# Performance work log

Hardware: AMD Instinct MI355X
Metric: run time of the kernel (lower is better)

The kernel has to match this reference:

```python
import jax, jax.numpy as jnp
import numpy as np

NEG_SLOPE = 0.01  # torch nn.LeakyReLU default


def setup_inputs() -> dict:
    key = jax.random.key(0)
    k1, k2, k3, k4, k5 = jax.random.split(key, 5)
    B, C, N, O = 32, 512, 1024, 512
    x = jax.random.normal(k1, (B, C, N), dtype=jnp.float32)
    wq = jax.random.normal(k2, (C,), dtype=jnp.float32) * (1.0 / np.sqrt(C))
    wk = jax.random.normal(k3, (C,), dtype=jnp.float32) * (1.0 / np.sqrt(C))
    wm = jax.random.normal(k4, (O, C), dtype=jnp.float32) * (1.0 / np.sqrt(C))
    bm = jax.random.normal(k5, (O,), dtype=jnp.float32) * 0.01
    return {"x": x, "wq": wq, "wk": wk, "wm": wm, "bm": bm}


def reference(x, wq, wk, wm, bm):
    # x: [B, C, N]
    q = jnp.einsum('c,bcn->bn', wq, x)            # [B, N] (Conv1d C->1, k=1, no bias)
    k = jnp.einsum('c,bcn->bn', wk, x)            # [B, N]
    scores = q[:, None, :] + k[:, :, None]        # [B, N, N] additive broadcast
    scores = jnp.where(scores > 0, scores, NEG_SLOPE * scores)  # LeakyReLU
    att = jax.nn.softmax(scores, axis=-1)         # softmax over last dim
    agg = jnp.einsum('bcn,bmn->bcm', x, att)      # weighted aggregation [B, C, N]
    out = jnp.einsum('oc,bcm->bom', wm, agg) + bm[None, :, None]  # Conv1d k=1
    return jax.nn.relu(out)
```

## Files before the change

kernel.cpp:

```cpp
#include <hip/hip_runtime.h>


constexpr int B = 32, C = 512, N = 1024, O = 512;
constexpr float L2E = 1.4426950408889634f;

typedef _Float16 half8 __attribute__((ext_vector_type(8)));
typedef _Float16 half4v __attribute__((ext_vector_type(4)));
typedef _Float16 half2v __attribute__((ext_vector_type(2)));
typedef float f32x4 __attribute__((ext_vector_type(4)));

#if __has_builtin(__builtin_amdgcn_exp2f)
#define EXP2(x) __builtin_amdgcn_exp2f(x)
#else
#define EXP2(x) exp2f(x)
#endif

__device__ __forceinline__ half8 cvt8(float4 a, float4 b) {
  half8 h;
  h[0] = (_Float16)a.x; h[1] = (_Float16)a.y; h[2] = (_Float16)a.z; h[3] = (_Float16)a.w;
  h[4] = (_Float16)b.x; h[5] = (_Float16)b.y; h[6] = (_Float16)b.z; h[7] = (_Float16)b.w;
  return h;
}

__global__ __launch_bounds__(256) void gemm_y_kernel(const float* __restrict__ x,
    const float* __restrict__ wm, const float* __restrict__ wq,
    const float* __restrict__ wk, float* __restrict__ q, float* __restrict__ k,
    _Float16* __restrict__ Yt) {
  __shared__ half2v Xs[16 * 130];
  __shared__ __align__(16) _Float16 Ws[128 * 40];
  int b  = blockIdx.y;
  int n0 = blockIdx.x * 128;
  int o0 = blockIdx.z * 128;
  int t = threadIdx.x;
  int w = t >> 6, l = t & 63;
  int nw = w >> 1, ow = w & 1;
  int lm = l & 15, q8 = (l >> 4) * 8, q4 = (l >> 4) * 4;

  int cp = t >> 4, ng = t & 15;
  int wrow = t >> 2, woff = (t & 3) * 8;
  bool doqk = (blockIdx.z == 0);
  float aq[8] = {}, ak[8] = {};

  f32x4 acc[4][4] = {};
  for (int c0 = 0; c0 < C; c0 += 32) {
    const float* xr = x + ((size_t)b * C + c0 + 2 * cp) * N + n0 + ng * 8;
    float4 a0 = *(const float4*)(xr);
    float4 a1 = *(const float4*)(xr + 4);
    float4 b0 = *(const float4*)(xr + N);
    float4 b1 = *(const float4*)(xr + N + 4);
    const float* wr = wm + (size_t)(o0 + wrow) * C + c0 + woff;
    float4 w0 = *(const float4*)(wr);
    float4 w1 = *(const float4*)(wr + 4);
    float4 w2 = *(const float4*)(wr + (size_t)64 * C);
    float4 w3 = *(const float4*)(wr + (size_t)64 * C + 4);

    if (doqk) {
      float2 wq2 = *(const float2*)&wq[c0 + 2 * cp];
      float2 wk2 = *(const float2*)&wk[c0 + 2 * cp];
      aq[0] = fmaf(wq2.x, a0.x, fmaf(wq2.y, b0.x, aq[0]));
      aq[1] = fmaf(wq2.x, a0.y, fmaf(wq2.y, b0.y, aq[1]));
      aq[2] = fmaf(wq2.x, a0.z, fmaf(wq2.y, b0.z, aq[2]));
      aq[3] = fmaf(wq2.x, a0.w, fmaf(wq2.y, b0.w, aq[3]));
      aq[4] = fmaf(wq2.x, a1.x, fmaf(wq2.y, b1.x, aq[4]));
      aq[5] = fmaf(wq2.x, a1.y, fmaf(wq2.y, b1.y, aq[5]));
      aq[6] = fmaf(wq2.x, a1.z, fmaf(wq2.y, b1.z, aq[6]));
      aq[7] = fmaf(wq2.x, a1.w, fmaf(wq2.y, b1.w, aq[7]));
      ak[0] = fmaf(wk2.x, a0.x, fmaf(wk2.y, b0.x, ak[0]));
      ak[1] = fmaf(wk2.x, a0.y, fmaf(wk2.y, b0.y, ak[1]));
      ak[2] = fmaf(wk2.x, a0.z, fmaf(wk2.y, b0.z, ak[2]));
      ak[3] = fmaf(wk2.x, a0.w, fmaf(wk2.y, b0.w, ak[3]));
      ak[4] = fmaf(wk2.x, a1.x, fmaf(wk2.y, b1.x, ak[4]));
      ak[5] = fmaf(wk2.x, a1.y, fmaf(wk2.y, b1.y, ak[5]));
      ak[6] = fmaf(wk2.x, a1.z, fmaf(wk2.y, b1.z, ak[6]));
      ak[7] = fmaf(wk2.x, a1.w, fmaf(wk2.y, b1.w, ak[7]));
    }

    __syncthreads();
    {
      half2v* xp = &Xs[cp * 130 + ng * 8];
      xp[0] = half2v{(_Float16)a0.x, (_Float16)b0.x};
      xp[1] = half2v{(_Float16)a0.y, (_Float16)b0.y};
      xp[2] = half2v{(_Float16)a0.z, (_Float16)b0.z};
      xp[3] = half2v{(_Float16)a0.w, (_Float16)b0.w};
      xp[4] = half2v{(_Float16)a1.x, (_Float16)b1.x};
      xp[5] = half2v{(_Float16)a1.y, (_Float16)b1.y};
      xp[6] = half2v{(_Float16)a1.z, (_Float16)b1.z};
      xp[7] = half2v{(_Float16)a1.w, (_Float16)b1.w};
      *(half8*)&Ws[wrow * 40 + woff]        = cvt8(w0, w1);
      *(half8*)&Ws[(wrow + 64) * 40 + woff] = cvt8(w2, w3);
    }
    __syncthreads();

    half8 af[4], bf[4];
#pragma unroll
    for (int i = 0; i < 4; ++i) {
      int nrow = nw * 64 + i * 16 + lm;
#pragma unroll
      for (int jp = 0; jp < 4; ++jp) {
        half2v p = Xs[(q4 + jp) * 130 + nrow];
        af[i][2 * jp]     = p[0];
        af[i][2 * jp + 1] = p[1];
      }
    }
#pragma unroll
    for (int j = 0; j < 4; ++j)
      bf[j] = *(const half8*)&Ws[(ow * 64 + j * 16 + lm) * 40 + q8];
#pragma unroll
    for (int i = 0; i < 4; ++i)
#pragma unroll
      for (int j = 0; j < 4; ++j)
        acc[i][j] = __builtin_amdgcn_mfma_f32_16x16x32_f16(af[i], bf[j], acc[i][j], 0, 0, 0);
  }

#pragma unroll
  for (int i = 0; i < 4; ++i) {
    int n_b = n0 + nw * 64 + i * 16 + (l >> 4) * 4;
#pragma unroll
    for (int j = 0; j < 4; ++j) {
      int o_c = o0 + ow * 64 + j * 16 + lm;
      half4v h;
      h[0] = (_Float16)acc[i][j][0];
      h[1] = (_Float16)acc[i][j][1];
      h[2] = (_Float16)acc[i][j][2];
      h[3] = (_Float16)acc[i][j][3];
      *(half4v*)&Yt[((size_t)b * O + o_c) * N + n_b] = h;
    }
  }

  if (doqk) {
    float* red = (float*)Ws;
    __syncthreads();
#pragma unroll
    for (int j = 0; j < 8; ++j) red[cp * 132 + ng * 8 + j] = aq[j];
    __syncthreads();
    if (t < 128) {
      float s = 0.f;
#pragma unroll
      for (int p = 0; p < 16; ++p) s += red[p * 132 + t];
      q[b * N + n0 + t] = L2E * s;
    }
    __syncthreads();
#pragma unroll
    for (int j = 0; j < 8; ++j) red[cp * 132 + ng * 8 + j] = ak[j];
    __syncthreads();
    if (t < 128) {
      float s = 0.f;
#pragma unroll
      for (int p = 0; p < 16; ++p) s += red[p * 132 + t];
      k[b * N + n0 + t] = L2E * s;
    }
  }
}

__global__ __launch_bounds__(256) void qmax_kernel(const float* __restrict__ q,
                                                   float* __restrict__ qmax) {
  int b = blockIdx.x;
  int tid = threadIdx.x;
  float m = -1e30f;
  for (int n = tid; n < N; n += 256) m = fmaxf(m, q[b * N + n]);
#pragma unroll
  for (int off = 32; off > 0; off >>= 1) m = fmaxf(m, __shfl_down(m, off, 64));
  __shared__ float red[4];
  if ((tid & 63) == 0) red[tid >> 6] = m;
  __syncthreads();
  if (tid == 0) qmax[b] = fmaxf(fmaxf(red[0], red[1]), fmaxf(red[2], red[3]));
}

__global__ __launch_bounds__(256) void gemm_out_kernel(const _Float16* __restrict__ Yt,
    const float* __restrict__ q, const float* __restrict__ k,
    const float* __restrict__ qmax, const float* __restrict__ bm,
    float* __restrict__ out) {
  __shared__ __align__(16) float qs[N];
  __shared__ float izs[128];
  int b  = blockIdx.y;
  int o0 = blockIdx.x * 128;
  int m0 = blockIdx.z * 128;
  int t = threadIdx.x;
  int w = t >> 6, l = t & 63;
  int mw = w >> 1, ow = w & 1;
  int lm = l & 15, g = l >> 4, q8 = g * 8;

  *(float4*)&qs[t * 4] = *(const float4*)&q[b * N + t * 4];

  float qmv = qmax[b];
  float k2[4], k3[4];
#pragma unroll
  for (int i = 0; i < 4; ++i) {
    float km = k[b * N + m0 + mw * 64 + i * 16 + lm];
    float s0 = qmv + km;
    float M  = fmaxf(s0, 0.01f * s0);
    k2[i] = km - M;
    k3[i] = fmaf(0.01f, km, -M);
  }
  float Zp[4] = {0.f, 0.f, 0.f, 0.f};
  const _Float16* ybase = Yt + ((size_t)b * O + o0 + ow * 64 + lm) * N + q8;
  __syncthreads();

  f32x4 acc[4][4] = {};
#pragma unroll 2
  for (int n0k = 0; n0k < N; n0k += 32) {
    half8 bf[4];
#pragma unroll
    for (int j = 0; j < 4; ++j)
      bf[j] = *(const half8*)(ybase + (size_t)(j * 16) * N + n0k);
    float4 qa = *(const float4*)&qs[n0k + q8];
    float4 qb = *(const float4*)&qs[n0k + q8 + 4];
    float qv[8] = {qa.x, qa.y, qa.z, qa.w, qb.x, qb.y, qb.z, qb.w};
#pragma unroll
    for (int i = 0; i < 4; ++i) {
      half8 af;
      float zz = 0.f;
#pragma unroll
      for (int jj = 0; jj < 8; ++jj) {
        float arg = fmaxf(qv[jj] + k2[i], fmaf(0.01f, qv[jj], k3[i]));
        float e = EXP2(arg);
        zz += e;
        af[jj] = (_Float16)e;
      }
      Zp[i] += zz;
#pragma unroll
      for (int j = 0; j < 4; ++j)
        acc[i][j] = __builtin_amdgcn_mfma_f32_16x16x32_f16(af, bf[j], acc[i][j], 0, 0, 0);
    }
  }

#pragma unroll
  for (int i = 0; i < 4; ++i) {
    float z = Zp[i];
    z += __shfl_xor(z, 16, 64);
    z += __shfl_xor(z, 32, 64);
    if (ow == 0 && g == 0) izs[mw * 64 + i * 16 + lm] = 1.0f / z;
  }
  __syncthreads();

#pragma unroll
  for (int i = 0; i < 4; ++i) {
    int m_b = m0 + mw * 64 + i * 16 + g * 4;
    float4 iz4 = *(const float4*)&izs[mw * 64 + i * 16 + g * 4];
#pragma unroll
    for (int j = 0; j < 4; ++j) {
      int o_c = o0 + ow * 64 + j * 16 + lm;
      float bias = bm[o_c];
      float4 r;
      r.x = fmaxf(fmaf(acc[i][j][0], iz4.x, bias), 0.f);
      r.y = fmaxf(fmaf(acc[i][j][1], iz4.y, bias), 0.f);
      r.z = fmaxf(fmaf(acc[i][j][2], iz4.z, bias), 0.f);
      r.w = fmaxf(fmaf(acc[i][j][3], iz4.w, bias), 0.f);
      *(float4*)&out[((size_t)b * O + o_c) * N + m_b] = r;
    }
  }
}

extern "C" void kernel_launch(void* const* d_in, const int* in_sizes, int n_in,
                              void* d_out, int out_size, void* d_ws, size_t ws_size,
                              hipStream_t stream) {
  const float* x  = (const float*)d_in[0];
  const float* wq = (const float*)d_in[1];
  const float* wk = (const float*)d_in[2];
  const float* wm = (const float*)d_in[3];
  const float* bm = (const float*)d_in[4];
  float* out = (float*)d_out;

  float* q    = (float*)d_ws;
  float* k    = q + B * N;
  float* qmax = k + B * N;
  _Float16* Yt = (_Float16*)(qmax + 64);

  gemm_y_kernel<<<dim3(N / 128, B, O / 128), 256, 0, stream>>>(x, wm, wq, wk, q, k, Yt);
  qmax_kernel<<<dim3(B), 256, 0, stream>>>(q, qmax);
  gemm_out_kernel<<<dim3(O / 128, B, N / 128), 256, 0, stream>>>(Yt, q, k, qmax, bm, out);
}
```

Before: 234.9 us.

## Stage Y tile in shared memory and split waves over m to cut redundant exp work

Changes the wave decomposition from a 2x2 (m,o) split to four waves each owning 32 m-rows across all 128 o-columns. Each exp/softmax weight is now computed once per block rather than twice, halving the transcendental work. The Y tile is staged cooperatively through padded shared memory each k-step, which adds two barriers per iteration and LDS traffic. The normalizer now sums the fp16-rounded weights so it matches what the MFMAs consume.

```diff
diff --git a/kernel.cpp b/kernel.cpp
--- a/kernel.cpp
+++ b/kernel.cpp
@@ -171,75 +171,84 @@
     const float* __restrict__ qmax, const float* __restrict__ bm,
     float* __restrict__ out) {
   __shared__ __align__(16) float qs[N];
+  __shared__ __align__(16) _Float16 Ys[128 * 40];
   __shared__ float izs[128];
   int b  = blockIdx.y;
   int o0 = blockIdx.x * 128;
   int m0 = blockIdx.z * 128;
   int t = threadIdx.x;
   int w = t >> 6, l = t & 63;
-  int mw = w >> 1, ow = w & 1;
   int lm = l & 15, g = l >> 4, q8 = g * 8;
 
   *(float4*)&qs[t * 4] = *(const float4*)&q[b * N + t * 4];
 
   float qmv = qmax[b];
-  float k2[4], k3[4];
-#pragma unroll
-  for (int i = 0; i < 4; ++i) {
-    float km = k[b * N + m0 + mw * 64 + i * 16 + lm];
+  float k2[2], k3[2];
+#pragma unroll
+  for (int i = 0; i < 2; ++i) {
+    float km = k[b * N + m0 + w * 32 + i * 16 + lm];
     float s0 = qmv + km;
     float M  = fmaxf(s0, 0.01f * s0);
     k2[i] = km - M;
     k3[i] = fmaf(0.01f, km, -M);
   }
-  float Zp[4] = {0.f, 0.f, 0.f, 0.f};
-  const _Float16* ybase = Yt + ((size_t)b * O + o0 + ow * 64 + lm) * N + q8;
+  float Zp[2] = {0.f, 0.f};
+  int yr = t >> 1, yp = t & 1;
+  const _Float16* ysrc = Yt + ((size_t)b * O + o0 + yr) * N + yp * 16;
   __syncthreads();
 
-  f32x4 acc[4][4] = {};
-#pragma unroll 2
+  f32x4 acc[2][8] = {};
   for (int n0k = 0; n0k < N; n0k += 32) {
-    half8 bf[4];
-#pragma unroll
-    for (int j = 0; j < 4; ++j)
-      bf[j] = *(const half8*)(ybase + (size_t)(j * 16) * N + n0k);
+    half8 y0 = *(const half8*)(ysrc + n0k);
+    half8 y1 = *(const half8*)(ysrc + n0k + 8);
     float4 qa = *(const float4*)&qs[n0k + q8];
     float4 qb = *(const float4*)&qs[n0k + q8 + 4];
     float qv[8] = {qa.x, qa.y, qa.z, qa.w, qb.x, qb.y, qb.z, qb.w};
-#pragma unroll
-    for (int i = 0; i < 4; ++i) {
-      half8 af;
+    half8 af[2];
+#pragma unroll
+    for (int i = 0; i < 2; ++i) {
       float zz = 0.f;
 #pragma unroll
       for (int jj = 0; jj < 8; ++jj) {
         float arg = fmaxf(qv[jj] + k2[i], fmaf(0.01f, qv[jj], k3[i]));
-        float e = EXP2(arg);
-        zz += e;
-        af[jj] = (_Float16)e;
+        _Float16 eh = (_Float16)EXP2(arg);
+        af[i][jj] = eh;
+        zz += (float)eh;
       }
       Zp[i] += zz;
-#pragma unroll
-      for (int j = 0; j < 4; ++j)
-        acc[i][j] = __builtin_amdgcn_mfma_f32_16x16x32_f16(af, bf[j], acc[i][j], 0, 0, 0);
-    }
-  }
-
-#pragma unroll
-  for (int i = 0; i < 4; ++i) {
+    }
+    __syncthreads();
+    *(half8*)&Ys[yr * 40 + yp * 16]     = y0;
+    *(half8*)&Ys[yr * 40 + yp * 16 + 8] = y1;
+    __syncthreads();
+
+    half8 bf[8];
+#pragma unroll
+    for (int j = 0; j < 8; ++j)
+      bf[j] = *(const half8*)&Ys[(j * 16 + lm) * 40 + q8];
+#pragma unroll
+    for (int i = 0; i < 2; ++i)
+#pragma unroll
+      for (int j = 0; j < 8; ++j)
+        acc[i][j] = __builtin_amdgcn_mfma_f32_16x16x32_f16(af[i], bf[j], acc[i][j], 0, 0, 0);
+  }
+
+#pragma unroll
+  for (int i = 0; i < 2; ++i) {
     float z = Zp[i];
     z += __shfl_xor(z, 16, 64);
     z += __shfl_xor(z, 32, 64);
-    if (ow == 0 && g == 0) izs[mw * 64 + i * 16 + lm] = 1.0f / z;
+    if (g == 0) izs[w * 32 + i * 16 + lm] = 1.0f / z;
   }
   __syncthreads();
 
 #pragma unroll
-  for (int i = 0; i < 4; ++i) {
-    int m_b = m0 + mw * 64 + i * 16 + g * 4;
-    float4 iz4 = *(const float4*)&izs[mw * 64 + i * 16 + g * 4];
-#pragma unroll
-    for (int j = 0; j < 4; ++j) {
-      int o_c = o0 + ow * 64 + j * 16 + lm;
+  for (int i = 0; i < 2; ++i) {
+    int m_b = m0 + w * 32 + i * 16 + g * 4;
+    float4 iz4 = *(const float4*)&izs[w * 32 + i * 16 + g * 4];
+#pragma unroll
+    for (int j = 0; j < 8; ++j) {
+      int o_c = o0 + j * 16 + lm;
       float bias = bm[o_c];
       float4 r;
       r.x = fmaxf(fmaf(acc[i][j][0], iz4.x, bias), 0.f);
```

Result: faster. 224.0 us (-4.6%).
